# Performance work log

Measured on AMD Instinct MI355X. Metric: run time of the kernel, lower is better.

Reference implementation:

```python
import jax, jax.numpy as jnp
import numpy as np

EPS = 1e-09  # present in module but unused in forward math

def setup_inputs() -> dict:
    key = jax.random.key(0)
    k1, k2 = jax.random.split(key)
    n, d = 4096, 512
    outputs = jax.random.normal(k1, (n, d), dtype=jnp.float32)
    labels = jax.random.randint(k2, (n,), 0, 100, dtype=jnp.int64)
    return {"outputs": outputs, "labels": labels, "margin": 1.0}

def reference(outputs, labels, margin):
    # Pairwise squared L2 distances D[i,j] = ||x_i - x_j||^2 via expansion.
    sq = jnp.sum(outputs * outputs, axis=-1)                     # [n]
    D = sq[:, None] + sq[None, :] - 2.0 * (outputs @ outputs.T)  # [n, n]
    D = jnp.maximum(D, 0.0)
    same = (labels[:, None] == labels[None, :])                  # [n, n] bool; includes diagonal
    zn1 = jnp.sum(same)
    zn2 = same.size - zn1
    sum1 = jnp.sum(jnp.where(same, D, 0.0))
    sum2 = jnp.sum(jnp.where(same, 0.0, jnp.maximum(0.0, margin - D)))
    return 0.5 * (sum1 / zn1 + sum2 / zn2)
```

## Files before the change

kernel.cpp:

```cpp
#include <hip/hip_runtime.h>
#include <stdint.h>

#define NROWS 4096
#define DIM   512
#define BK    32
#define TILE  128
#define NBLK  32
#define NPAIR 528

typedef float f32x4 __attribute__((ext_vector_type(4)));
typedef short s16x8 __attribute__((ext_vector_type(8)));

#define OFF_XB   0u
#define OFF_SQ   (NROWS * DIM * 2u)
#define OFF_LAB  (OFF_SQ + NROWS * 4u)
#define OFF_ACC  (OFF_LAB + NROWS * 4u)

__device__ __forceinline__ unsigned short f2bf(float f) {
  unsigned u = __float_as_uint(f);
  return (unsigned short)((u + 0x7FFFu + ((u >> 16) & 1u)) >> 16);
}

typedef __attribute__((address_space(1))) unsigned int glb_uint;
typedef __attribute__((address_space(3))) unsigned int lds_uint;

__device__ __forceinline__ void gl2lds16(const void* g, void* l) {
  __builtin_amdgcn_global_load_lds(
      (glb_uint*)(uintptr_t)g,
      (lds_uint*)(unsigned int)(uintptr_t)l,
      16, 0, 0);
}

__global__ __launch_bounds__(256) void prep_kernel(
    const float* __restrict__ X, const long long* __restrict__ lab,
    unsigned short* __restrict__ Xb, float* __restrict__ sq,
    int* __restrict__ labi, float* __restrict__ accum)
{
  int t = threadIdx.x;
  int gid = blockIdx.x * 256 + t;
  if (gid < 4) accum[gid] = 0.0f;
  if (gid < NROWS) labi[gid] = (int)lab[gid];

  int wave = t >> 6, lane = t & 63;
  int row = blockIdx.x * 4 + wave;
  const float4* Xr = (const float4*)(X + (size_t)row * DIM);
  float4 a = Xr[lane * 2];
  float4 b = Xr[lane * 2 + 1];

  uint4 pk;
  pk.x = (unsigned)f2bf(a.x) | ((unsigned)f2bf(a.y) << 16);
  pk.y = (unsigned)f2bf(a.z) | ((unsigned)f2bf(a.w) << 16);
  pk.z = (unsigned)f2bf(b.x) | ((unsigned)f2bf(b.y) << 16);
  pk.w = (unsigned)f2bf(b.z) | ((unsigned)f2bf(b.w) << 16);
  *(uint4*)(Xb + (size_t)row * DIM + lane * 8) = pk;

  float s = a.x*a.x + a.y*a.y + a.z*a.z + a.w*a.w
          + b.x*b.x + b.y*b.y + b.z*b.z + b.w*b.w;
  #pragma unroll
  for (int off = 32; off; off >>= 1) s += __shfl_down(s, off, 64);
  if (lane == 0) sq[row] = s;
}

__global__ __launch_bounds__(256) void pair_kernel(
    const unsigned short* __restrict__ Xb, const float* __restrict__ sq,
    const int* __restrict__ labi, const float* __restrict__ marginp,
    float* __restrict__ accum)
{
  __shared__ unsigned short As[TILE * BK];
  __shared__ unsigned short Bs[TILE * BK];
  __shared__ float sRow[TILE], sCol[TILE];
  __shared__ int   lRow[TILE], lCol[TILE];
  __shared__ float rs1[4], rs2[4];
  __shared__ int   rc[4];

  int t = threadIdx.x;

  int rem = blockIdx.x, bi = 0;
  while (rem >= (NBLK - bi)) { rem -= (NBLK - bi); bi++; }
  int bj = bi + rem;

  int wave = t >> 6, lane = t & 63;
  int quad = lane >> 4, ml = lane & 15;
  int waveRow = (wave >> 1) * 64, waveCol = (wave & 1) * 64;

  f32x4 acc[4][4] = {};

  const int r0 = t >> 2;
  const int c0 = (t & 3) * 8;
  const size_t gA0 = (size_t)(bi * TILE +       r0) * DIM + c0;
  const size_t gA1 = (size_t)(bi * TILE + 64 +  r0) * DIM + c0;
  const size_t gB0 = (size_t)(bj * TILE +       r0) * DIM + c0;
  const size_t gB1 = (size_t)(bj * TILE + 64 +  r0) * DIM + c0;

  const s16x8* Ap = (const s16x8*)As;
  const s16x8* Bp = (const s16x8*)Bs;

  for (int kt = 0; kt < DIM / BK; ++kt) {
    __syncthreads();
    size_t ko = (size_t)kt * BK;
    gl2lds16(Xb + gA0 + ko, (void*)(As + t * 8));
    gl2lds16(Xb + gA1 + ko, (void*)(As + 2048 + t * 8));
    gl2lds16(Xb + gB0 + ko, (void*)(Bs + t * 8));
    gl2lds16(Xb + gB1 + ko, (void*)(Bs + 2048 + t * 8));
    __syncthreads();

    s16x8 af[4], bfr[4];
    #pragma unroll
    for (int r = 0; r < 4; ++r)
      af[r] = Ap[(waveRow + r * 16 + ml) * 4 + quad];
    #pragma unroll
    for (int c = 0; c < 4; ++c)
      bfr[c] = Bp[(waveCol + c * 16 + ml) * 4 + quad];

    #pragma unroll
    for (int r = 0; r < 4; ++r)
      #pragma unroll
      for (int c = 0; c < 4; ++c)
        acc[r][c] = __builtin_amdgcn_mfma_f32_16x16x32_bf16(af[r], bfr[c], acc[r][c], 0, 0, 0);
  }

  if (t < TILE) {
    sRow[t] = sq[bi * TILE + t];
    lRow[t] = labi[bi * TILE + t];
  } else {
    int u = t - TILE;
    sCol[u] = sq[bj * TILE + u];
    lCol[u] = labi[bj * TILE + u];
  }
  __syncthreads();

  float margin = *marginp;
  float s1 = 0.f, s2 = 0.f;
  int cnt = 0;
  #pragma unroll
  for (int c = 0; c < 4; ++c) {
    int col = waveCol + c * 16 + ml;
    float sqc = sCol[col];
    int lc = lCol[col];
    #pragma unroll
    for (int r = 0; r < 4; ++r) {
      int rbase = waveRow + r * 16 + quad * 4;
      #pragma unroll
      for (int i = 0; i < 4; ++i) {
        int row = rbase + i;
        float d = sRow[row] + sqc - 2.0f * acc[r][c][i];
        d = fmaxf(d, 0.0f);
        if (lRow[row] == lc) { s1 += d; cnt++; }
        else                 { s2 += fmaxf(margin - d, 0.0f); }
      }
    }
  }

  #pragma unroll
  for (int off = 32; off; off >>= 1) {
    s1  += __shfl_down(s1, off, 64);
    s2  += __shfl_down(s2, off, 64);
    cnt += __shfl_down(cnt, off, 64);
  }
  if (lane == 0) { rs1[wave] = s1; rs2[wave] = s2; rc[wave] = cnt; }
  __syncthreads();
  if (t == 0) {
    float f = (bi == bj) ? 1.f : 2.f;
    float S1 = 0.f, S2 = 0.f;
    int C = 0;
    for (int w = 0; w < 4; ++w) { S1 += rs1[w]; S2 += rs2[w]; C += rc[w]; }
    atomicAdd(&accum[0], S1 * f);
    atomicAdd(&accum[1], S2 * f);
    atomicAdd((unsigned*)accum + 2, (unsigned)C * (unsigned)((bi == bj) ? 1 : 2));
  }
}

__global__ void final_kernel(const float* __restrict__ accum, float* __restrict__ out) {
  unsigned c1 = ((const unsigned*)accum)[2];
  double zn1 = (double)c1;
  double zn2 = (double)NROWS * (double)NROWS - zn1;
  double res = 0.5 * ((double)accum[0] / zn1 + (double)accum[1] / zn2);
  out[0] = (float)res;
}

extern "C" void kernel_launch(void* const* d_in, const int* in_sizes, int n_in,
                              void* d_out, int out_size, void* d_ws, size_t ws_size,
                              hipStream_t stream) {
  const float*     X      = (const float*)d_in[0];
  const long long* lab    = (const long long*)d_in[1];
  const float*     margin = (const float*)d_in[2];
  float*           out    = (float*)d_out;

  char* ws = (char*)d_ws;
  unsigned short* Xb   = (unsigned short*)(ws + OFF_XB);
  float*          sq   = (float*)(ws + OFF_SQ);
  int*            labi = (int*)(ws + OFF_LAB);
  float*          accum= (float*)(ws + OFF_ACC);

  prep_kernel<<<NROWS / 4, 256, 0, stream>>>(X, lab, Xb, sq, labi, accum);
  pair_kernel<<<NPAIR, 256, 0, stream>>>(Xb, sq, labi, margin, accum);
  final_kernel<<<1, 1, 0, stream>>>(accum, out);
}
```

Measured before the change: 98.06 us.

## Double-buffer LDS tiles, fuse final reduction via last-block counter, prefetch row metadata

Splits the GEMM K-loop into a two-stage LDS ping-pong so the global-to-LDS load of the next K slice is issued before the MFMAs on the current slice, leaving one barrier per step instead of two. The LDS tile layout changes to a chunk-major arrangement, which alters the LDS access pattern. Squared norms and labels are loaded into registers at kernel start. The separate final kernel is removed and replaced by a last-block-done atomic counter that computes the output, which adds a fence and an extra atomic per block.

```diff
diff --git a/kernel.cpp b/kernel.cpp
--- a/kernel.cpp
+++ b/kernel.cpp
@@ -7,6 +7,7 @@
 #define TILE  128
 #define NBLK  32
 #define NPAIR 528
+#define KSTEPS (DIM / BK)
 
 typedef float f32x4 __attribute__((ext_vector_type(4)));
 typedef short s16x8 __attribute__((ext_vector_type(8)));
@@ -64,10 +65,10 @@
 __global__ __launch_bounds__(256) void pair_kernel(
     const unsigned short* __restrict__ Xb, const float* __restrict__ sq,
     const int* __restrict__ labi, const float* __restrict__ marginp,
-    float* __restrict__ accum)
+    float* __restrict__ accum, float* __restrict__ out)
 {
-  __shared__ unsigned short As[TILE * BK];
-  __shared__ unsigned short Bs[TILE * BK];
+  __shared__ unsigned short As[2][4096];
+  __shared__ unsigned short Bs[2][4096];
   __shared__ float sRow[TILE], sCol[TILE];
   __shared__ int   lRow[TILE], lCol[TILE];
   __shared__ float rs1[4], rs2[4];
@@ -83,53 +84,65 @@
   int quad = lane >> 4, ml = lane & 15;
   int waveRow = (wave >> 1) * 64, waveCol = (wave & 1) * 64;
 
+  float margin = *marginp;
+  float sqv; int lbv;
+  {
+    int u = t & 127;
+    int base = (t < TILE ? bi : bj) * TILE + u;
+    sqv = sq[base];
+    lbv = labi[base];
+  }
+
+  const int rr = t & 127;
+  const int ch = t >> 7;
+  const size_t gA = (size_t)(bi * TILE + rr) * DIM + ch * 8;
+  const size_t gB = (size_t)(bj * TILE + rr) * DIM + ch * 8;
+
   f32x4 acc[4][4] = {};
 
-  const int r0 = t >> 2;
-  const int c0 = (t & 3) * 8;
-  const size_t gA0 = (size_t)(bi * TILE +       r0) * DIM + c0;
-  const size_t gA1 = (size_t)(bi * TILE + 64 +  r0) * DIM + c0;
-  const size_t gB0 = (size_t)(bj * TILE +       r0) * DIM + c0;
-  const size_t gB1 = (size_t)(bj * TILE + 64 +  r0) * DIM + c0;
-
-  const s16x8* Ap = (const s16x8*)As;
-  const s16x8* Bp = (const s16x8*)Bs;
-
-  for (int kt = 0; kt < DIM / BK; ++kt) {
+  #define STAGE(buf, kt)                                                      \
+    do {                                                                      \
+      size_t ko = (size_t)(kt) * BK;                                          \
+      gl2lds16(Xb + gA + ko,      (void*)(&As[(buf)][t * 8]));                \
+      gl2lds16(Xb + gA + ko + 16, (void*)(&As[(buf)][2048 + t * 8]));         \
+      gl2lds16(Xb + gB + ko,      (void*)(&Bs[(buf)][t * 8]));                \
+      gl2lds16(Xb + gB + ko + 16, (void*)(&Bs[(buf)][2048 + t * 8]));         \
+    } while (0)
+
+  #define COMPUTE(buf)                                                        \
+    do {                                                                      \
+      const s16x8* Ap = (const s16x8*)As[(buf)];                              \
+      const s16x8* Bp = (const s16x8*)Bs[(buf)];                              \
+      s16x8 af[4], bfr[4];                                                    \
+      _Pragma("unroll")                                                       \
+      for (int r = 0; r < 4; ++r)                                             \
+        af[r] = Ap[quad * 128 + waveRow + r * 16 + ml];                       \
+      _Pragma("unroll")                                                       \
+      for (int c = 0; c < 4; ++c)                                             \
+        bfr[c] = Bp[quad * 128 + waveCol + c * 16 + ml];                      \
+      _Pragma("unroll")                                                       \
+      for (int r = 0; r < 4; ++r)                                             \
+        _Pragma("unroll")                                                     \
+        for (int c = 0; c < 4; ++c)                                           \
+          acc[r][c] = __builtin_amdgcn_mfma_f32_16x16x32_bf16(                \
+              af[r], bfr[c], acc[r][c], 0, 0, 0);                             \
+    } while (0)
+
+  STAGE(0, 0);
+  int cur = 0;
+  for (int kt = 0; kt < KSTEPS - 1; ++kt) {
     __syncthreads();
-    size_t ko = (size_t)kt * BK;
-    gl2lds16(Xb + gA0 + ko, (void*)(As + t * 8));
-    gl2lds16(Xb + gA1 + ko, (void*)(As + 2048 + t * 8));
-    gl2lds16(Xb + gB0 + ko, (void*)(Bs + t * 8));
-    gl2lds16(Xb + gB1 + ko, (void*)(Bs + 2048 + t * 8));
-    __syncthreads();
-
-    s16x8 af[4], bfr[4];
-    #pragma unroll
-    for (int r = 0; r < 4; ++r)
-      af[r] = Ap[(waveRow + r * 16 + ml) * 4 + quad];
-    #pragma unroll
-    for (int c = 0; c < 4; ++c)
-      bfr[c] = Bp[(waveCol + c * 16 + ml) * 4 + quad];
-
-    #pragma unroll
-    for (int r = 0; r < 4; ++r)
-      #pragma unroll
-      for (int c = 0; c < 4; ++c)
-        acc[r][c] = __builtin_amdgcn_mfma_f32_16x16x32_bf16(af[r], bfr[c], acc[r][c], 0, 0, 0);
-  }
-
-  if (t < TILE) {
-    sRow[t] = sq[bi * TILE + t];
-    lRow[t] = labi[bi * TILE + t];
-  } else {
-    int u = t - TILE;
-    sCol[u] = sq[bj * TILE + u];
-    lCol[u] = labi[bj * TILE + u];
+    STAGE(cur ^ 1, kt + 1);
+    COMPUTE(cur);
+    cur ^= 1;
   }
   __syncthreads();
-
-  float margin = *marginp;
+  COMPUTE(cur);
+
+  if (t < TILE) { sRow[t] = sqv; lRow[t] = lbv; }
+  else          { sCol[t - TILE] = sqv; lCol[t - TILE] = lbv; }
+  __syncthreads();
+
   float s1 = 0.f, s2 = 0.f;
   int cnt = 0;
   #pragma unroll
@@ -167,15 +180,20 @@
     atomicAdd(&accum[0], S1 * f);
     atomicAdd(&accum[1], S2 * f);
     atomicAdd((unsigned*)accum + 2, (unsigned)C * (unsigned)((bi == bj) ? 1 : 2));
-  }
-}
-
-__global__ void final_kernel(const float* __restrict__ accum, float* __restrict__ out) {
-  unsigned c1 = ((const unsigned*)accum)[2];
-  double zn1 = (double)c1;
-  double zn2 = (double)NROWS * (double)NROWS - zn1;
-  double res = 0.5 * ((double)accum[0] / zn1 + (double)accum[1] / zn2);
-  out[0] = (float)res;
+    __threadfence();
+    unsigned done = atomicAdd((unsigned*)accum + 3, 1u);
+    if (done == NPAIR - 1) {
+      __threadfence();
+      float S1f = atomicAdd(&accum[0], 0.0f);
+      float S2f = atomicAdd(&accum[1], 0.0f);
+      unsigned c1 = atomicAdd((unsigned*)accum + 2, 0u);
+      double zn1 = (double)c1;
+      double zn2 = (double)NROWS * (double)NROWS - zn1;
+      out[0] = (float)(0.5 * ((double)S1f / zn1 + (double)S2f / zn2));
+    }
+  }
+  #undef STAGE
+  #undef COMPUTE
 }
 
 extern "C" void kernel_launch(void* const* d_in, const int* in_sizes, int n_in,
@@ -193,6 +211,5 @@
   float*          accum= (float*)(ws + OFF_ACC);
 
   prep_kernel<<<NROWS / 4, 256, 0, stream>>>(X, lab, Xb, sq, labi, accum);
-  pair_kernel<<<NPAIR, 256, 0, stream>>>(Xb, sq, labi, margin, accum);
-  final_kernel<<<1, 1, 0, stream>>>(accum, out);
-}
+  pair_kernel<<<NPAIR, 256, 0, stream>>>(Xb, sq, labi, margin, accum, out);
+}
```

Result: slower. 116.4 us (+18.7%).

## Load MFMA operands directly from global memory and fold final reduction into pair kernel

Applied to the files above, without the earlier changes.

Removes the LDS staging and both barriers per k-step: each wave now reads its bf16 A/B fragments straight from global memory (L2/cache-resident, 4 MB matrix) into registers, unrolled by 4 so loads can be issued ahead. Per-row norms and labels are read from global instead of shared memory. The separate final kernel is replaced by a last-block-done atomic counter that computes the output, saving one launch. The cost is that operand reuse across waves now goes through cache rather than LDS, so global traffic per block rises, and the loads are strided 16-byte accesses per lane.

```diff
diff --git a/kernel.cpp b/kernel.cpp
--- a/kernel.cpp
+++ b/kernel.cpp
@@ -3,10 +3,10 @@
 
 #define NROWS 4096
 #define DIM   512
-#define BK    32
 #define TILE  128
 #define NBLK  32
 #define NPAIR 528
+#define KSTEPS 16
 
 typedef float f32x4 __attribute__((ext_vector_type(4)));
 typedef short s16x8 __attribute__((ext_vector_type(8)));
@@ -19,16 +19,6 @@
 __device__ __forceinline__ unsigned short f2bf(float f) {
   unsigned u = __float_as_uint(f);
   return (unsigned short)((u + 0x7FFFu + ((u >> 16) & 1u)) >> 16);
-}
-
-typedef __attribute__((address_space(1))) unsigned int glb_uint;
-typedef __attribute__((address_space(3))) unsigned int lds_uint;
-
-__device__ __forceinline__ void gl2lds16(const void* g, void* l) {
-  __builtin_amdgcn_global_load_lds(
-      (glb_uint*)(uintptr_t)g,
-      (lds_uint*)(unsigned int)(uintptr_t)l,
-      16, 0, 0);
 }
 
 __global__ __launch_bounds__(256) void prep_kernel(
@@ -64,12 +54,8 @@
 __global__ __launch_bounds__(256) void pair_kernel(
     const unsigned short* __restrict__ Xb, const float* __restrict__ sq,
     const int* __restrict__ labi, const float* __restrict__ marginp,
-    float* __restrict__ accum)
+    float* __restrict__ accum, float* __restrict__ out)
 {
-  __shared__ unsigned short As[TILE * BK];
-  __shared__ unsigned short Bs[TILE * BK];
-  __shared__ float sRow[TILE], sCol[TILE];
-  __shared__ int   lRow[TILE], lCol[TILE];
   __shared__ float rs1[4], rs2[4];
   __shared__ int   rc[4];
 
@@ -81,71 +67,50 @@
 
   int wave = t >> 6, lane = t & 63;
   int quad = lane >> 4, ml = lane & 15;
-  int waveRow = (wave >> 1) * 64, waveCol = (wave & 1) * 64;
+  int rowBase = bi * TILE + (wave >> 1) * 64;
+  int colBase = bj * TILE + (wave & 1) * 64;
+
+  float margin = *marginp;
+
+  const size_t aBase = (size_t)(rowBase + ml) * DIM + quad * 8;
+  const size_t bBase = (size_t)(colBase + ml) * DIM + quad * 8;
 
   f32x4 acc[4][4] = {};
 
-  const int r0 = t >> 2;
-  const int c0 = (t & 3) * 8;
-  const size_t gA0 = (size_t)(bi * TILE +       r0) * DIM + c0;
-  const size_t gA1 = (size_t)(bi * TILE + 64 +  r0) * DIM + c0;
-  const size_t gB0 = (size_t)(bj * TILE +       r0) * DIM + c0;
-  const size_t gB1 = (size_t)(bj * TILE + 64 +  r0) * DIM + c0;
-
-  const s16x8* Ap = (const s16x8*)As;
-  const s16x8* Bp = (const s16x8*)Bs;
-
-  for (int kt = 0; kt < DIM / BK; ++kt) {
-    __syncthreads();
-    size_t ko = (size_t)kt * BK;
-    gl2lds16(Xb + gA0 + ko, (void*)(As + t * 8));
-    gl2lds16(Xb + gA1 + ko, (void*)(As + 2048 + t * 8));
-    gl2lds16(Xb + gB0 + ko, (void*)(Bs + t * 8));
-    gl2lds16(Xb + gB1 + ko, (void*)(Bs + 2048 + t * 8));
-    __syncthreads();
-
+  #pragma unroll 4
+  for (int kt = 0; kt < KSTEPS; ++kt) {
+    const int ko = kt * 32;
     s16x8 af[4], bfr[4];
     #pragma unroll
     for (int r = 0; r < 4; ++r)
-      af[r] = Ap[(waveRow + r * 16 + ml) * 4 + quad];
+      af[r] = *(const s16x8*)(Xb + aBase + (size_t)r * 16 * DIM + ko);
     #pragma unroll
     for (int c = 0; c < 4; ++c)
-      bfr[c] = Bp[(waveCol + c * 16 + ml) * 4 + quad];
-
+      bfr[c] = *(const s16x8*)(Xb + bBase + (size_t)c * 16 * DIM + ko);
     #pragma unroll
     for (int r = 0; r < 4; ++r)
       #pragma unroll
       for (int c = 0; c < 4; ++c)
-        acc[r][c] = __builtin_amdgcn_mfma_f32_16x16x32_bf16(af[r], bfr[c], acc[r][c], 0, 0, 0);
+        acc[r][c] = __builtin_amdgcn_mfma_f32_16x16x32_bf16(
+            af[r], bfr[c], acc[r][c], 0, 0, 0);
   }
 
-  if (t < TILE) {
-    sRow[t] = sq[bi * TILE + t];
-    lRow[t] = labi[bi * TILE + t];
-  } else {
-    int u = t - TILE;
-    sCol[u] = sq[bj * TILE + u];
-    lCol[u] = labi[bj * TILE + u];
-  }
-  __syncthreads();
-
-  float margin = *marginp;
   float s1 = 0.f, s2 = 0.f;
   int cnt = 0;
   #pragma unroll
   for (int c = 0; c < 4; ++c) {
-    int col = waveCol + c * 16 + ml;
-    float sqc = sCol[col];
-    int lc = lCol[col];
+    int col = colBase + c * 16 + ml;
+    float sqc = sq[col];
+    int lc = labi[col];
     #pragma unroll
     for (int r = 0; r < 4; ++r) {
-      int rbase = waveRow + r * 16 + quad * 4;
+      int rbase = rowBase + r * 16 + quad * 4;
       #pragma unroll
       for (int i = 0; i < 4; ++i) {
         int row = rbase + i;
-        float d = sRow[row] + sqc - 2.0f * acc[r][c][i];
+        float d = sq[row] + sqc - 2.0f * acc[r][c][i];
         d = fmaxf(d, 0.0f);
-        if (lRow[row] == lc) { s1 += d; cnt++; }
+        if (labi[row] == lc) { s1 += d; cnt++; }
         else                 { s2 += fmaxf(margin - d, 0.0f); }
       }
     }
@@ -167,15 +132,18 @@
     atomicAdd(&accum[0], S1 * f);
     atomicAdd(&accum[1], S2 * f);
     atomicAdd((unsigned*)accum + 2, (unsigned)C * (unsigned)((bi == bj) ? 1 : 2));
+    __threadfence();
+    unsigned done = atomicAdd((unsigned*)accum + 3, 1u);
+    if (done == NPAIR - 1) {
+      __threadfence();
+      float S1f = atomicAdd(&accum[0], 0.0f);
+      float S2f = atomicAdd(&accum[1], 0.0f);
+      unsigned c1 = atomicAdd((unsigned*)accum + 2, 0u);
+      double zn1 = (double)c1;
+      double zn2 = (double)NROWS * (double)NROWS - zn1;
+      out[0] = (float)(0.5 * ((double)S1f / zn1 + (double)S2f / zn2));
+    }
   }
-}
-
-__global__ void final_kernel(const float* __restrict__ accum, float* __restrict__ out) {
-  unsigned c1 = ((const unsigned*)accum)[2];
-  double zn1 = (double)c1;
-  double zn2 = (double)NROWS * (double)NROWS - zn1;
-  double res = 0.5 * ((double)accum[0] / zn1 + (double)accum[1] / zn2);
-  out[0] = (float)res;
 }
 
 extern "C" void kernel_launch(void* const* d_in, const int* in_sizes, int n_in,
@@ -193,6 +161,5 @@
   float*          accum= (float*)(ws + OFF_ACC);
 
   prep_kernel<<<NROWS / 4, 256, 0, stream>>>(X, lab, Xb, sq, labi, accum);
-  pair_kernel<<<NPAIR, 256, 0, stream>>>(Xb, sq, labi, margin, accum);
-  final_kernel<<<1, 1, 0, stream>>>(accum, out);
+  pair_kernel<<<NPAIR, 256, 0, stream>>>(Xb, sq, labi, margin, accum, out);
 }
```

Measured after the change: 122.4 us. 24.8% more time.

## Compute full tile grid with XCD-aware mapping and fuse final reduction via last-block

Applied to the files above, without the earlier changes.

Replaces the upper-triangular 528-tile launch with all 1024 tiles, remapping block ids so neighbouring tiles land on the same XCD. It also removes the final kernel: the last block to finish, detected through an atomic counter, computes the output. Per-row norms and labels are now loaded before the GEMM loop so their latency is hidden. The cost is nearly double the MFMA work, since the symmetric half is no longer skipped, in exchange for better load balance and one fewer launch.

```diff
diff --git a/kernel.cpp b/kernel.cpp
--- a/kernel.cpp
+++ b/kernel.cpp
@@ -6,7 +6,8 @@
 #define BK    32
 #define TILE  128
 #define NBLK  32
-#define NPAIR 528
+#define NTILE 1024
+#define KSTEPS (DIM / BK)
 
 typedef float f32x4 __attribute__((ext_vector_type(4)));
 typedef short s16x8 __attribute__((ext_vector_type(8)));
@@ -64,7 +65,7 @@
 __global__ __launch_bounds__(256) void pair_kernel(
     const unsigned short* __restrict__ Xb, const float* __restrict__ sq,
     const int* __restrict__ labi, const float* __restrict__ marginp,
-    float* __restrict__ accum)
+    float* __restrict__ accum, float* __restrict__ out)
 {
   __shared__ unsigned short As[TILE * BK];
   __shared__ unsigned short Bs[TILE * BK];
@@ -75,15 +76,22 @@
 
   int t = threadIdx.x;
 
-  int rem = blockIdx.x, bi = 0;
-  while (rem >= (NBLK - bi)) { rem -= (NBLK - bi); bi++; }
-  int bj = bi + rem;
+  int wgid = (blockIdx.x & 7) * (NTILE / 8) + (blockIdx.x >> 3);
+  int bi = wgid >> 5;
+  int bj = wgid & 31;
 
   int wave = t >> 6, lane = t & 63;
   int quad = lane >> 4, ml = lane & 15;
   int waveRow = (wave >> 1) * 64, waveCol = (wave & 1) * 64;
 
-  f32x4 acc[4][4] = {};
+  float margin = *marginp;
+  float sqv; int lbv;
+  {
+    int u = t & 127;
+    int base = (t < TILE ? bi : bj) * TILE + u;
+    sqv = sq[base];
+    lbv = labi[base];
+  }
 
   const int r0 = t >> 2;
   const int c0 = (t & 3) * 8;
@@ -95,7 +103,9 @@
   const s16x8* Ap = (const s16x8*)As;
   const s16x8* Bp = (const s16x8*)Bs;
 
-  for (int kt = 0; kt < DIM / BK; ++kt) {
+  f32x4 acc[4][4] = {};
+
+  for (int kt = 0; kt < KSTEPS; ++kt) {
     __syncthreads();
     size_t ko = (size_t)kt * BK;
     gl2lds16(Xb + gA0 + ko, (void*)(As + t * 8));
@@ -119,17 +129,10 @@
         acc[r][c] = __builtin_amdgcn_mfma_f32_16x16x32_bf16(af[r], bfr[c], acc[r][c], 0, 0, 0);
   }
 
-  if (t < TILE) {
-    sRow[t] = sq[bi * TILE + t];
-    lRow[t] = labi[bi * TILE + t];
-  } else {
-    int u = t - TILE;
-    sCol[u] = sq[bj * TILE + u];
-    lCol[u] = labi[bj * TILE + u];
-  }
+  if (t < TILE) { sRow[t] = sqv; lRow[t] = lbv; }
+  else          { sCol[t - TILE] = sqv; lCol[t - TILE] = lbv; }
   __syncthreads();
 
-  float margin = *marginp;
   float s1 = 0.f, s2 = 0.f;
   int cnt = 0;
   #pragma unroll
@@ -160,22 +163,24 @@
   if (lane == 0) { rs1[wave] = s1; rs2[wave] = s2; rc[wave] = cnt; }
   __syncthreads();
   if (t == 0) {
-    float f = (bi == bj) ? 1.f : 2.f;
     float S1 = 0.f, S2 = 0.f;
     int C = 0;
     for (int w = 0; w < 4; ++w) { S1 += rs1[w]; S2 += rs2[w]; C += rc[w]; }
-    atomicAdd(&accum[0], S1 * f);
-    atomicAdd(&accum[1], S2 * f);
-    atomicAdd((unsigned*)accum + 2, (unsigned)C * (unsigned)((bi == bj) ? 1 : 2));
-  }
-}
-
-__global__ void final_kernel(const float* __restrict__ accum, float* __restrict__ out) {
-  unsigned c1 = ((const unsigned*)accum)[2];
-  double zn1 = (double)c1;
-  double zn2 = (double)NROWS * (double)NROWS - zn1;
-  double res = 0.5 * ((double)accum[0] / zn1 + (double)accum[1] / zn2);
-  out[0] = (float)res;
+    atomicAdd(&accum[0], S1);
+    atomicAdd(&accum[1], S2);
+    atomicAdd((unsigned*)accum + 2, (unsigned)C);
+    __threadfence();
+    unsigned done = atomicAdd((unsigned*)accum + 3, 1u);
+    if (done == NTILE - 1) {
+      __threadfence();
+      float S1f = atomicAdd(&accum[0], 0.0f);
+      float S2f = atomicAdd(&accum[1], 0.0f);
+      unsigned c1 = atomicAdd((unsigned*)accum + 2, 0u);
+      double zn1 = (double)c1;
+      double zn2 = (double)NROWS * (double)NROWS - zn1;
+      out[0] = (float)(0.5 * ((double)S1f / zn1 + (double)S2f / zn2));
+    }
+  }
 }
 
 extern "C" void kernel_launch(void* const* d_in, const int* in_sizes, int n_in,
@@ -193,6 +198,5 @@
   float*          accum= (float*)(ws + OFF_ACC);
 
   prep_kernel<<<NROWS / 4, 256, 0, stream>>>(X, lab, Xb, sq, labi, accum);
-  pair_kernel<<<NPAIR, 256, 0, stream>>>(Xb, sq, labi, margin, accum);
-  final_kernel<<<1, 1, 0, stream>>>(accum, out);
-}
+  pair_kernel<<<NTILE, 256, 0, stream>>>(Xb, sq, labi, margin, accum, out);
+}
```

Measured after the change: 131.3 us. 1.34x slower.
